# Performance work log

Hardware: AMD Instinct MI355X
Metric: run time of the kernel (lower is better)

The kernel has to match this reference:

```python
import jax, jax.numpy as jnp
import numpy as np

B, N, D, H = 2, 512, 256, 8
HD = D // H
DFF = 4 * D
EPS = 1e-5


def layer_norm(x, g, b):
    m = jnp.mean(x, axis=-1, keepdims=True)
    v = jnp.mean(jnp.square(x - m), axis=-1, keepdims=True)
    return (x - m) * jax.lax.rsqrt(v + EPS) * g + b


def setup_inputs() -> dict:
    key = jax.random.key(0)
    ks = jax.random.split(key, 16)
    s = 0.02
    return {
        "node_features": jax.random.normal(ks[0], (B, N, D), jnp.float32),
        "edge_features": jax.random.normal(ks[1], (B, N, N, D), jnp.float32),
        "adjacency_mask": jax.random.randint(ks[2], (B, N, N), 0, 2, jnp.int32),
        "node_norm_g": jnp.ones((D,), jnp.float32),
        "node_norm_b": jnp.zeros((D,), jnp.float32),
        "edge_norm_g": jnp.ones((D,), jnp.float32),
        "edge_norm_b": jnp.zeros((D,), jnp.float32),
        "Wq": jax.random.normal(ks[3], (D, D), jnp.float32) * s,
        "bq": jnp.zeros((D,), jnp.float32),
        "Wk": jax.random.normal(ks[4], (D, D), jnp.float32) * s,
        "bk": jnp.zeros((D,), jnp.float32),
        "Wv": jax.random.normal(ks[5], (D, D), jnp.float32) * s,
        "bv": jnp.zeros((D,), jnp.float32),
        "Wo": jax.random.normal(ks[6], (D, D), jnp.float32) * s,
        "bo": jnp.zeros((D,), jnp.float32),
        "We": jax.random.normal(ks[7], (D, H), jnp.float32) * s,
        "be": jnp.zeros((H,), jnp.float32),
        "ff_norm_g": jnp.ones((D,), jnp.float32),
        "ff_norm_b": jnp.zeros((D,), jnp.float32),
        "W1": jax.random.normal(ks[8], (D, DFF), jnp.float32) * s,
        "b1": jnp.zeros((DFF,), jnp.float32),
        "W2": jax.random.normal(ks[9], (DFF, D), jnp.float32) * s,
        "b2": jnp.zeros((D,), jnp.float32),
    }


def reference(node_features, edge_features, adjacency_mask,
              node_norm_g, node_norm_b, edge_norm_g, edge_norm_b,
              Wq, bq, Wk, bk, Wv, bv, Wo, bo, We, be,
              ff_norm_g, ff_norm_b, W1, b1, W2, b2):
    x = node_features
    nn_ = layer_norm(x, node_norm_g, node_norm_b)
    # project and split heads: (B, H, N, HD)
    q = (nn_ @ Wq + bq).reshape(B, N, H, HD).transpose(0, 2, 1, 3)
    k = (nn_ @ Wk + bk).reshape(B, N, H, HD).transpose(0, 2, 1, 3)
    v = (nn_ @ Wv + bv).reshape(B, N, H, HD).transpose(0, 2, 1, 3)
    scores = jnp.einsum('bhnd,bhmd->bhnm', q, k) / jnp.sqrt(jnp.float32(HD))
    # edge bias: LayerNorm over D then Linear(D->H), move H first
    eb = layer_norm(edge_features, edge_norm_g, edge_norm_b) @ We + be  # (B,N,N,H)
    scores = scores + eb.transpose(0, 3, 1, 2)
    scores = jnp.where(adjacency_mask[:, None, :, :] == 0, -jnp.inf, scores)
    attn = jax.nn.softmax(scores, axis=-1)
    out = jnp.einsum('bhnm,bhmd->bhnd', attn, v)
    out = out.transpose(0, 2, 1, 3).reshape(B, N, D) @ Wo + bo
    x = x + out
    # feedforward (dropout is identity at inference)
    h = layer_norm(x, ff_norm_g, ff_norm_b)
    h = jax.nn.gelu(h @ W1 + b1, approximate=False) @ W2 + b2
    return x + h
```

## Files before the change

### kernel.cpp

```cpp
#include <hip/hip_runtime.h>
#include <hip/hip_bf16.h>

typedef unsigned int uint;

constexpr float EPS_ = 1e-5f;

#define DEV __device__ __forceinline__

DEV float gelu_(float x){ return 0.5f*x*(1.f + erff(x*0.70710678118654752f)); }

__global__ __launch_bounds__(256) void k_setup(
    const float* __restrict__ g, const float* __restrict__ b,
    const float* __restrict__ We, const float* __restrict__ be,
    float* __restrict__ GW, float* __restrict__ A, float* __restrict__ C)
{
    const int d = threadIdx.x;
    __shared__ float redA[256*8];
    __shared__ float redC[256*8];
    float gd = g[d], bd = b[d];
    #pragma unroll
    for (int h = 0; h < 8; ++h) {
        float w = We[d*8+h];
        float gw = gd*w;
        GW[d*8+h] = gw;
        redA[d*8+h] = gw;
        redC[d*8+h] = bd*w;
    }
    __syncthreads();
    for (int s = 128; s >= 1; s >>= 1) {
        if (d < s) {
            #pragma unroll
            for (int h = 0; h < 8; ++h) {
                redA[d*8+h] += redA[(d+s)*8+h];
                redC[d*8+h] += redC[(d+s)*8+h];
            }
        }
        __syncthreads();
    }
    if (d < 8) {
        A[d] = redA[d];
        C[d] = redC[d] + be[d];
    }
}

__global__ __launch_bounds__(256) void k_qkv(
    const float* __restrict__ x,
    const float* __restrict__ g, const float* __restrict__ bta,
    const float* __restrict__ Wq, const float* __restrict__ bq,
    const float* __restrict__ Wk, const float* __restrict__ bk,
    const float* __restrict__ Wv, const float* __restrict__ bv,
    float* __restrict__ q, float* __restrict__ k, float* __restrict__ v)
{
    const int t = threadIdx.x;
    const int wid = t >> 6, l = t & 63;
    const int r0 = blockIdx.x << 1;
    __shared__ float sxT[256*2];
    if (wid < 2) {
        const int row = r0 + wid;
        const float4 xv4 = ((const float4*)x)[row*64 + l];
        float s  = xv4.x + xv4.y + xv4.z + xv4.w;
        float q2 = xv4.x*xv4.x + xv4.y*xv4.y + xv4.z*xv4.z + xv4.w*xv4.w;
        #pragma unroll
        for (int o = 32; o >= 1; o >>= 1) { s += __shfl_xor(s, o); q2 += __shfl_xor(q2, o); }
        const float m = s * (1.f/256.f);
        const float rinv = rsqrtf(q2*(1.f/256.f) - m*m + EPS_);
        const float4 g4 = ((const float4*)g)[l];
        const float4 b4 = ((const float4*)bta)[l];
        sxT[(4*l+0)*2 + wid] = (xv4.x - m)*rinv*g4.x + b4.x;
        sxT[(4*l+1)*2 + wid] = (xv4.y - m)*rinv*g4.y + b4.y;
        sxT[(4*l+2)*2 + wid] = (xv4.z - m)*rinv*g4.z + b4.z;
        sxT[(4*l+3)*2 + wid] = (xv4.w - m)*rinv*g4.w + b4.w;
    }
    __syncthreads();
    float aq0 = bq[t], ak0 = bk[t], av0 = bv[t];
    float aq1 = aq0, ak1 = ak0, av1 = av0;
    for (int d = 0; d < 256; d += 2) {
        const float4 s4 = *((const float4*)&sxT[d*2]);
        const float wqa = Wq[d*256 + t], wqb = Wq[(d+1)*256 + t];
        const float wka = Wk[d*256 + t], wkb = Wk[(d+1)*256 + t];
        const float wva = Wv[d*256 + t], wvb = Wv[(d+1)*256 + t];
        aq0 = fmaf(s4.x, wqa, aq0); aq0 = fmaf(s4.z, wqb, aq0);
        aq1 = fmaf(s4.y, wqa, aq1); aq1 = fmaf(s4.w, wqb, aq1);
        ak0 = fmaf(s4.x, wka, ak0); ak0 = fmaf(s4.z, wkb, ak0);
        ak1 = fmaf(s4.y, wka, ak1); ak1 = fmaf(s4.w, wkb, ak1);
        av0 = fmaf(s4.x, wva, av0); av0 = fmaf(s4.z, wvb, av0);
        av1 = fmaf(s4.y, wva, av1); av1 = fmaf(s4.w, wvb, av1);
    }
    q[(r0+0)*256 + t] = aq0; q[(r0+1)*256 + t] = aq1;
    k[(r0+0)*256 + t] = ak0; k[(r0+1)*256 + t] = ak1;
    v[(r0+0)*256 + t] = av0; v[(r0+1)*256 + t] = av1;
}

__global__ __launch_bounds__(256) void k_eattn(
    const float4* __restrict__ ep,
    const int*   __restrict__ msk,
    const float* __restrict__ GWg, const float* __restrict__ Avec, const float* __restrict__ Cvec,
    const float* __restrict__ qg, const float4* __restrict__ kg4, const float* __restrict__ vg,
    float* __restrict__ ao)
{
    __shared__ float slds[256*20];
    __shared__ float sb[8*512];
    __shared__ float sqv[256];
    __shared__ float sden[8];
    const int t = threadIdx.x;
    const int bi = blockIdx.x;
    const int b = bi >> 9;
    sqv[t] = qg[(size_t)bi*256 + t] * 0.17677669529663687f;
    __syncthreads();

    for (int half = 0; half < 2; ++half) {
        const long long rowBase = ((long long)bi << 9) + (half << 8);
        const int krow0 = (b << 9) + (half << 8);
        float sum = 0.f, ssq = 0.f;
        float S[8]  = {0.f,0.f,0.f,0.f,0.f,0.f,0.f,0.f};
        float qk[8] = {0.f,0.f,0.f,0.f,0.f,0.f,0.f,0.f};

        for (int c = 0; c < 16; ++c) {
            #pragma unroll
            for (int kk = 0; kk < 4; ++kk) {
                const int l2 = (kk << 8) + t;
                const int r = l2 >> 2, u = l2 & 3;
                *((float4*)&slds[r*20 + (u << 2)]) = ep[(rowBase + r)*64 + (c << 2) + u];
            }
            __syncthreads();
            const float* srow = &slds[t*20];
            const int d0 = c << 4;
            #pragma unroll
            for (int j4 = 0; j4 < 4; ++j4) {
                const float4 e4 = *((const float4*)&srow[j4 << 2]);
                #pragma unroll
                for (int u = 0; u < 4; ++u) {
                    const float e = (u==0) ? e4.x : (u==1) ? e4.y : (u==2) ? e4.z : e4.w;
                    const float* gw = &GWg[(size_t)(d0 + (j4 << 2) + u) << 3];
                    sum += e;
                    ssq = fmaf(e, e, ssq);
                    S[0] = fmaf(e, gw[0], S[0]); S[1] = fmaf(e, gw[1], S[1]);
                    S[2] = fmaf(e, gw[2], S[2]); S[3] = fmaf(e, gw[3], S[3]);
                    S[4] = fmaf(e, gw[4], S[4]); S[5] = fmaf(e, gw[5], S[5]);
                    S[6] = fmaf(e, gw[6], S[6]); S[7] = fmaf(e, gw[7], S[7]);
                }
            }
            __syncthreads();
        }

        for (int c = 0; c < 16; ++c) {
            #pragma unroll
            for (int kk = 0; kk < 4; ++kk) {
                const int l2 = (kk << 8) + t;
                const int r = l2 >> 2, u = l2 & 3;
                *((float4*)&slds[r*20 + (u << 2)]) = kg4[(size_t)(krow0 + r)*64 + (c << 2) + u];
            }
            __syncthreads();
            const float* srow = &slds[t*20];
            const float4* q4p = (const float4*)&sqv[c << 4];
            float acc = qk[c >> 1];
            #pragma unroll
            for (int j4 = 0; j4 < 4; ++j4) {
                const float4 k4 = *((const float4*)&srow[j4 << 2]);
                const float4 q4 = q4p[j4];
                acc = fmaf(k4.x, q4.x, acc); acc = fmaf(k4.y, q4.y, acc);
                acc = fmaf(k4.z, q4.z, acc); acc = fmaf(k4.w, q4.w, acc);
            }
            qk[c >> 1] = acc;
            __syncthreads();
        }

        const float m = sum * (1.f/256.f);
        const float rinv = rsqrtf(ssq*(1.f/256.f) - m*m + EPS_);
        const float mb = (msk[rowBase + t] == 0) ? -1e30f : 0.f;
        const int jrow = (half << 8) + t;
        #pragma unroll
        for (int h = 0; h < 8; ++h)
            sb[h*512 + jrow] = qk[h] + rinv * (S[h] - m * Avec[h]) + Cvec[h] + mb;
    }
    __syncthreads();

    {
        const int h = t >> 5, l = t & 31;
        float* base = &sb[h*512 + (l << 4)];
        float4 s4[4];
        float pmax = -3.0e38f;
        #pragma unroll
        for (int i = 0; i < 4; ++i) {
            s4[i] = *((const float4*)&base[i << 2]);
            pmax = fmaxf(pmax, fmaxf(fmaxf(s4[i].x, s4[i].y), fmaxf(s4[i].z, s4[i].w)));
        }
        #pragma unroll
        for (int o = 16; o >= 1; o >>= 1) pmax = fmaxf(pmax, __shfl_xor(pmax, o));
        float psum = 0.f;
        #pragma unroll
        for (int i = 0; i < 4; ++i) {
            const float p0 = __expf(s4[i].x - pmax), p1 = __expf(s4[i].y - pmax);
            const float p2 = __expf(s4[i].z - pmax), p3 = __expf(s4[i].w - pmax);
            psum += (p0 + p1) + (p2 + p3);
            *((float4*)&base[i << 2]) = make_float4(p0, p1, p2, p3);
        }
        #pragma unroll
        for (int o = 16; o >= 1; o >>= 1) psum += __shfl_xor(psum, o);
        if (l == 0) sden[h] = psum;
    }
    __syncthreads();

    {
        const int h = t >> 5;
        const float* vb = vg + ((size_t)b << 9)*256 + t;
        const float4* spr4 = (const float4*)&sb[h*512];
        float a0 = 0.f, a1 = 0.f, a2 = 0.f, a3 = 0.f;
        for (int j4 = 0; j4 < 128; ++j4) {
            const float4 p4 = spr4[j4];
            const float* vj = vb + ((size_t)j4 << 2)*256;
            a0 = fmaf(p4.x, vj[0],   a0);
            a1 = fmaf(p4.y, vj[256], a1);
            a2 = fmaf(p4.z, vj[512], a2);
            a3 = fmaf(p4.w, vj[768], a3);
        }
        ao[(size_t)bi*256 + t] = (a0+a1+a2+a3) / sden[h];
    }
}

__global__ __launch_bounds__(256) void k_proj(
    const float* __restrict__ at, const float* __restrict__ Wo,
    const float* __restrict__ bo, const float* __restrict__ x,
    float* __restrict__ x1)
{
    const int t = threadIdx.x;
    const int wid = t >> 6, l = t & 63;
    const int r0 = blockIdx.x << 1;
    __shared__ float saT[256*2];
    if (wid < 2) {
        const float4 a4 = ((const float4*)at)[(r0 + wid)*64 + l];
        saT[(4*l+0)*2 + wid] = a4.x;
        saT[(4*l+1)*2 + wid] = a4.y;
        saT[(4*l+2)*2 + wid] = a4.z;
        saT[(4*l+3)*2 + wid] = a4.w;
    }
    __syncthreads();
    float A0 = bo[t], A1 = A0;
    for (int d = 0; d < 256; d += 2) {
        const float4 s4 = *((const float4*)&saT[d*2]);
        const float wa = Wo[d*256 + t], wb = Wo[(d+1)*256 + t];
        A0 = fmaf(s4.x, wa, A0); A0 = fmaf(s4.z, wb, A0);
        A1 = fmaf(s4.y, wa, A1); A1 = fmaf(s4.w, wb, A1);
    }
    x1[(r0+0)*256 + t] = A0 + x[(r0+0)*256 + t];
    x1[(r0+1)*256 + t] = A1 + x[(r0+1)*256 + t];
}

__global__ __launch_bounds__(256) void k_ff(
    const float* __restrict__ x1, const float* __restrict__ g,
    const float* __restrict__ bb,
    const float* __restrict__ W1, const float* __restrict__ b1,
    const float* __restrict__ W2, const float* __restrict__ b2,
    float* __restrict__ out)
{
    const int t = threadIdx.x;
    const int wid = t >> 6, l = t & 63;
    const int r0 = blockIdx.x << 2;
    __shared__ float shT[256*4];
    __shared__ float sfT[1024*4];
    {
        const int row = r0 + wid;
        const float4 xv4 = ((const float4*)x1)[row*64 + l];
        float s  = xv4.x + xv4.y + xv4.z + xv4.w;
        float q2 = xv4.x*xv4.x + xv4.y*xv4.y + xv4.z*xv4.z + xv4.w*xv4.w;
        #pragma unroll
        for (int o = 32; o >= 1; o >>= 1) { s += __shfl_xor(s, o); q2 += __shfl_xor(q2, o); }
        const float m = s * (1.f/256.f);
        const float rinv = rsqrtf(q2*(1.f/256.f) - m*m + EPS_);
        const float4 g4 = ((const float4*)g)[l];
        const float4 b4 = ((const float4*)bb)[l];
        shT[(4*l+0)*4 + wid] = (xv4.x - m)*rinv*g4.x + b4.x;
        shT[(4*l+1)*4 + wid] = (xv4.y - m)*rinv*g4.y + b4.y;
        shT[(4*l+2)*4 + wid] = (xv4.z - m)*rinv*g4.z + b4.z;
        shT[(4*l+3)*4 + wid] = (xv4.w - m)*rinv*g4.w + b4.w;
    }
    __syncthreads();
    const float4 bc = ((const float4*)b1)[t];
    float4 Ac0 = make_float4(bc.x,bc.x,bc.x,bc.x);
    float4 Ac1 = make_float4(bc.y,bc.y,bc.y,bc.y);
    float4 Ac2 = make_float4(bc.z,bc.z,bc.z,bc.z);
    float4 Ac3 = make_float4(bc.w,bc.w,bc.w,bc.w);
    const float4* W14 = (const float4*)W1;
    for (int d = 0; d < 256; ++d) {
        const float4 s4 = *((const float4*)&shT[d*4]);
        const float4 w4 = W14[d*256 + t];
        Ac0.x = fmaf(s4.x, w4.x, Ac0.x); Ac0.y = fmaf(s4.y, w4.x, Ac0.y);
        Ac0.z = fmaf(s4.z, w4.x, Ac0.z); Ac0.w = fmaf(s4.w, w4.x, Ac0.w);
        Ac1.x = fmaf(s4.x, w4.y, Ac1.x); Ac1.y = fmaf(s4.y, w4.y, Ac1.y);
        Ac1.z = fmaf(s4.z, w4.y, Ac1.z); Ac1.w = fmaf(s4.w, w4.y, Ac1.w);
        Ac2.x = fmaf(s4.x, w4.z, Ac2.x); Ac2.y = fmaf(s4.y, w4.z, Ac2.y);
        Ac2.z = fmaf(s4.z, w4.z, Ac2.z); Ac2.w = fmaf(s4.w, w4.z, Ac2.w);
        Ac3.x = fmaf(s4.x, w4.w, Ac3.x); Ac3.y = fmaf(s4.y, w4.w, Ac3.y);
        Ac3.z = fmaf(s4.z, w4.w, Ac3.z); Ac3.w = fmaf(s4.w, w4.w, Ac3.w);
    }
    *((float4*)&sfT[(4*t+0)*4]) = make_float4(gelu_(Ac0.x), gelu_(Ac0.y), gelu_(Ac0.z), gelu_(Ac0.w));
    *((float4*)&sfT[(4*t+1)*4]) = make_float4(gelu_(Ac1.x), gelu_(Ac1.y), gelu_(Ac1.z), gelu_(Ac1.w));
    *((float4*)&sfT[(4*t+2)*4]) = make_float4(gelu_(Ac2.x), gelu_(Ac2.y), gelu_(Ac2.z), gelu_(Ac2.w));
    *((float4*)&sfT[(4*t+3)*4]) = make_float4(gelu_(Ac3.x), gelu_(Ac3.y), gelu_(Ac3.z), gelu_(Ac3.w));
    __syncthreads();
    const float b2v = b2[t];
    float4 AO = make_float4(b2v,b2v,b2v,b2v);
    for (int kk = 0; kk < 1024; ++kk) {
        const float4 s4 = *((const float4*)&sfT[kk*4]);
        const float w = W2[kk*256 + t];
        AO.x = fmaf(s4.x, w, AO.x); AO.y = fmaf(s4.y, w, AO.y);
        AO.z = fmaf(s4.z, w, AO.z); AO.w = fmaf(s4.w, w, AO.w);
    }
    out[(r0+0)*256 + t] = AO.x + x1[(r0+0)*256 + t];
    out[(r0+1)*256 + t] = AO.y + x1[(r0+1)*256 + t];
    out[(r0+2)*256 + t] = AO.z + x1[(r0+2)*256 + t];
    out[(r0+3)*256 + t] = AO.w + x1[(r0+3)*256 + t];
}

extern "C" void kernel_launch(void* const* d_in, const int* in_sizes, int n_in,
                              void* d_out, int out_size, void* d_ws, size_t ws_size,
                              hipStream_t stream) {
    const float* x   = (const float*)d_in[0];
    const float* ef  = (const float*)d_in[1];
    const int*   am  = (const int*)d_in[2];
    const float* ng  = (const float*)d_in[3];
    const float* nb  = (const float*)d_in[4];
    const float* eg  = (const float*)d_in[5];
    const float* ebb = (const float*)d_in[6];
    const float* Wq  = (const float*)d_in[7];
    const float* bq  = (const float*)d_in[8];
    const float* Wk  = (const float*)d_in[9];
    const float* bk  = (const float*)d_in[10];
    const float* Wv  = (const float*)d_in[11];
    const float* bv  = (const float*)d_in[12];
    const float* Wo  = (const float*)d_in[13];
    const float* bo  = (const float*)d_in[14];
    const float* We  = (const float*)d_in[15];
    const float* be  = (const float*)d_in[16];
    const float* fg  = (const float*)d_in[17];
    const float* fb  = (const float*)d_in[18];
    const float* W1  = (const float*)d_in[19];
    const float* b1  = (const float*)d_in[20];
    const float* W2  = (const float*)d_in[21];
    const float* b2  = (const float*)d_in[22];

    float* ws  = (float*)d_ws;
    float* GW  = ws;
    float* Av  = ws + 2048;
    float* Cv  = ws + 2064;
    float* q   = ws + 4096;
    float* k   = q  + 262144;
    float* v   = k  + 262144;
    float* ao  = v  + 262144;
    float* x1  = ao + 262144;

    hipLaunchKernelGGL(k_setup, dim3(1), dim3(256), 0, stream, eg, ebb, We, be, GW, Av, Cv);
    hipLaunchKernelGGL(k_qkv, dim3(512), dim3(256), 0, stream,
                       x, ng, nb, Wq, bq, Wk, bk, Wv, bv, q, k, v);
    hipLaunchKernelGGL(k_eattn, dim3(1024), dim3(256), 0, stream,
                       (const float4*)ef, am, GW, Av, Cv, q, (const float4*)k, v, ao);
    hipLaunchKernelGGL(k_proj, dim3(512), dim3(256), 0, stream, ao, Wo, bo, x, x1);
    hipLaunchKernelGGL(k_ff, dim3(256), dim3(256), 0, stream,
                       x1, fg, fb, W1, b1, W2, b2, (float*)d_out);
}
```

Before: 293.0 us.

## Prefetch next edge/key chunk into registers while computing current chunk

Merges the edge-feature and key loops into one 32-step loop and software-pipelines the global loads. Each step issues the next chunk's float4 loads into registers before computing on the current LDS tile, so global latency overlaps the FMA work. The cost is extra live registers and a per-iteration branch, which could reduce occupancy.

Result: no change. 291.6 us (-0.5%).

```diff
diff --git a/kernel.cpp b/kernel.cpp
--- a/kernel.cpp
+++ b/kernel.cpp
@@ -108,6 +108,8 @@
     sqv[t] = qg[(size_t)bi*256 + t] * 0.17677669529663687f;
     __syncthreads();
 
+    const int r = t >> 2, u = t & 3;
+
     for (int half = 0; half < 2; ++half) {
         const long long rowBase = ((long long)bi << 9) + (half << 8);
         const int krow0 = (b << 9) + (half << 8);
@@ -115,53 +117,65 @@
         float S[8]  = {0.f,0.f,0.f,0.f,0.f,0.f,0.f,0.f};
         float qk[8] = {0.f,0.f,0.f,0.f,0.f,0.f,0.f,0.f};
 
-        for (int c = 0; c < 16; ++c) {
-            #pragma unroll
-            for (int kk = 0; kk < 4; ++kk) {
-                const int l2 = (kk << 8) + t;
-                const int r = l2 >> 2, u = l2 & 3;
-                *((float4*)&slds[r*20 + (u << 2)]) = ep[(rowBase + r)*64 + (c << 2) + u];
-            }
+        float4 R0, R1, R2, R3;
+        {
+            R0 = ep[(rowBase + r      )*64 + u];
+            R1 = ep[(rowBase + r +  64)*64 + u];
+            R2 = ep[(rowBase + r + 128)*64 + u];
+            R3 = ep[(rowBase + r + 192)*64 + u];
+        }
+        for (int cc = 0; cc < 32; ++cc) {
+            *((float4*)&slds[(r      )*20 + (u << 2)]) = R0;
+            *((float4*)&slds[(r +  64)*20 + (u << 2)]) = R1;
+            *((float4*)&slds[(r + 128)*20 + (u << 2)]) = R2;
+            *((float4*)&slds[(r + 192)*20 + (u << 2)]) = R3;
             __syncthreads();
-            const float* srow = &slds[t*20];
-            const int d0 = c << 4;
-            #pragma unroll
-            for (int j4 = 0; j4 < 4; ++j4) {
-                const float4 e4 = *((const float4*)&srow[j4 << 2]);
-                #pragma unroll
-                for (int u = 0; u < 4; ++u) {
-                    const float e = (u==0) ? e4.x : (u==1) ? e4.y : (u==2) ? e4.z : e4.w;
-                    const float* gw = &GWg[(size_t)(d0 + (j4 << 2) + u) << 3];
-                    sum += e;
-                    ssq = fmaf(e, e, ssq);
-                    S[0] = fmaf(e, gw[0], S[0]); S[1] = fmaf(e, gw[1], S[1]);
-                    S[2] = fmaf(e, gw[2], S[2]); S[3] = fmaf(e, gw[3], S[3]);
-                    S[4] = fmaf(e, gw[4], S[4]); S[5] = fmaf(e, gw[5], S[5]);
-                    S[6] = fmaf(e, gw[6], S[6]); S[7] = fmaf(e, gw[7], S[7]);
+            if (cc + 1 < 32) {
+                const int nc = cc + 1;
+                if (nc < 16) {
+                    R0 = ep[(rowBase + r      )*64 + (nc << 2) + u];
+                    R1 = ep[(rowBase + r +  64)*64 + (nc << 2) + u];
+                    R2 = ep[(rowBase + r + 128)*64 + (nc << 2) + u];
+                    R3 = ep[(rowBase + r + 192)*64 + (nc << 2) + u];
+                } else {
+                    const int kc = nc - 16;
+                    R0 = kg4[(size_t)(krow0 + r      )*64 + (kc << 2) + u];
+                    R1 = kg4[(size_t)(krow0 + r +  64)*64 + (kc << 2) + u];
+                    R2 = kg4[(size_t)(krow0 + r + 128)*64 + (kc << 2) + u];
+                    R3 = kg4[(size_t)(krow0 + r + 192)*64 + (kc << 2) + u];
                 }
             }
-            __syncthreads();
-        }
-
-        for (int c = 0; c < 16; ++c) {
-            #pragma unroll
-            for (int kk = 0; kk < 4; ++kk) {
-                const int l2 = (kk << 8) + t;
-                const int r = l2 >> 2, u = l2 & 3;
-                *((float4*)&slds[r*20 + (u << 2)]) = kg4[(size_t)(krow0 + r)*64 + (c << 2) + u];
+            const float* srow = &slds[t*20];
+            if (cc < 16) {
+                const int d0 = cc << 4;
+                #pragma unroll
+                for (int j4 = 0; j4 < 4; ++j4) {
+                    const float4 e4 = *((const float4*)&srow[j4 << 2]);
+                    #pragma unroll
+                    for (int uu = 0; uu < 4; ++uu) {
+                        const float e = (uu==0) ? e4.x : (uu==1) ? e4.y : (uu==2) ? e4.z : e4.w;
+                        const float* gw = &GWg[(size_t)(d0 + (j4 << 2) + uu) << 3];
+                        sum += e;
+                        ssq = fmaf(e, e, ssq);
+                        S[0] = fmaf(e, gw[0], S[0]); S[1] = fmaf(e, gw[1], S[1]);
+                        S[2] = fmaf(e, gw[2], S[2]); S[3] = fmaf(e, gw[3], S[3]);
+                        S[4] = fmaf(e, gw[4], S[4]); S[5] = fmaf(e, gw[5], S[5]);
+                        S[6] = fmaf(e, gw[6], S[6]); S[7] = fmaf(e, gw[7], S[7]);
+                    }
+                }
+            } else {
+                const int kc = cc - 16;
+                const float4* q4p = (const float4*)&sqv[kc << 4];
+                float acc = qk[kc >> 1];
+                #pragma unroll
+                for (int j4 = 0; j4 < 4; ++j4) {
+                    const float4 k4 = *((const float4*)&srow[j4 << 2]);
+                    const float4 q4 = q4p[j4];
+                    acc = fmaf(k4.x, q4.x, acc); acc = fmaf(k4.y, q4.y, acc);
+                    acc = fmaf(k4.z, q4.z, acc); acc = fmaf(k4.w, q4.w, acc);
+                }
+                qk[kc >> 1] = acc;
             }
-            __syncthreads();
-            const float* srow = &slds[t*20];
-            const float4* q4p = (const float4*)&sqv[c << 4];
-            float acc = qk[c >> 1];
-            #pragma unroll
-            for (int j4 = 0; j4 < 4; ++j4) {
-                const float4 k4 = *((const float4*)&srow[j4 << 2]);
-                const float4 q4 = q4p[j4];
-                acc = fmaf(k4.x, q4.x, acc); acc = fmaf(k4.y, q4.y, acc);
-                acc = fmaf(k4.z, q4.z, acc); acc = fmaf(k4.w, q4.w, acc);
-            }
-            qk[c >> 1] = acc;
             __syncthreads();
         }
 
@@ -172,8 +186,8 @@
         #pragma unroll
         for (int h = 0; h < 8; ++h)
             sb[h*512 + jrow] = qk[h] + rinv * (S[h] - m * Avec[h]) + Cvec[h] + mb;
-    }
-    __syncthreads();
+        __syncthreads();
+    }
 
     {
         const int h = t >> 5, l = t & 31;
```

## Fold setup into QKV kernel, fuse proj+FF, share LDS in edge attention

Applied to the files above, without the earlier changes.

The one-block setup kernel is folded into block 0 of the QKV kernel, using a wave-shuffle reduction instead of a shared-memory tree. The output projection and feedforward kernels are fused so x1 stays in LDS, with the FF now processing 2 rows per block instead of 4. In the edge-attention kernel, the staging buffer and the score buffer share one LDS array and launch bounds request 5 blocks per CU, aiming for higher occupancy. Risks: fewer rows per block in the FF doubles the W1/W2 weight reads, and the S/qk state from both halves is now held in registers at the same time.

Result: faster. 271.8 us (median of 3 runs) (-7.2%).

```diff
diff --git a/kernel.cpp b/kernel.cpp
--- a/kernel.cpp
+++ b/kernel.cpp
@@ -8,40 +8,6 @@
 #define DEV __device__ __forceinline__
 
 DEV float gelu_(float x){ return 0.5f*x*(1.f + erff(x*0.70710678118654752f)); }
-
-__global__ __launch_bounds__(256) void k_setup(
-    const float* __restrict__ g, const float* __restrict__ b,
-    const float* __restrict__ We, const float* __restrict__ be,
-    float* __restrict__ GW, float* __restrict__ A, float* __restrict__ C)
-{
-    const int d = threadIdx.x;
-    __shared__ float redA[256*8];
-    __shared__ float redC[256*8];
-    float gd = g[d], bd = b[d];
-    #pragma unroll
-    for (int h = 0; h < 8; ++h) {
-        float w = We[d*8+h];
-        float gw = gd*w;
-        GW[d*8+h] = gw;
-        redA[d*8+h] = gw;
-        redC[d*8+h] = bd*w;
-    }
-    __syncthreads();
-    for (int s = 128; s >= 1; s >>= 1) {
-        if (d < s) {
-            #pragma unroll
-            for (int h = 0; h < 8; ++h) {
-                redA[d*8+h] += redA[(d+s)*8+h];
-                redC[d*8+h] += redC[(d+s)*8+h];
-            }
-        }
-        __syncthreads();
-    }
-    if (d < 8) {
-        A[d] = redA[d];
-        C[d] = redC[d] + be[d];
-    }
-}
 
 __global__ __launch_bounds__(256) void k_qkv(
     const float* __restrict__ x,
@@ -49,9 +15,45 @@
     const float* __restrict__ Wq, const float* __restrict__ bq,
     const float* __restrict__ Wk, const float* __restrict__ bk,
     const float* __restrict__ Wv, const float* __restrict__ bv,
+    const float* __restrict__ eg, const float* __restrict__ ebb,
+    const float* __restrict__ We, const float* __restrict__ be,
+    float* __restrict__ GW, float* __restrict__ Av, float* __restrict__ Cv,
     float* __restrict__ q, float* __restrict__ k, float* __restrict__ v)
 {
     const int t = threadIdx.x;
+    __shared__ float redA2[4][8];
+    __shared__ float redC2[4][8];
+    if (blockIdx.x == 0) {
+        float gd = eg[t], bd = ebb[t];
+        float a_loc[8], c_loc[8];
+        #pragma unroll
+        for (int h = 0; h < 8; ++h) {
+            float w = We[t*8 + h];
+            float gw = gd * w;
+            GW[t*8 + h] = gw;
+            a_loc[h] = gw;
+            c_loc[h] = bd * w;
+        }
+        #pragma unroll
+        for (int h = 0; h < 8; ++h) {
+            #pragma unroll
+            for (int o = 32; o >= 1; o >>= 1) {
+                a_loc[h] += __shfl_xor(a_loc[h], o);
+                c_loc[h] += __shfl_xor(c_loc[h], o);
+            }
+        }
+        if ((t & 63) == 0) {
+            const int w = t >> 6;
+            #pragma unroll
+            for (int h = 0; h < 8; ++h) { redA2[w][h] = a_loc[h]; redC2[w][h] = c_loc[h]; }
+        }
+        __syncthreads();
+        if (t < 8) {
+            Av[t] = redA2[0][t] + redA2[1][t] + redA2[2][t] + redA2[3][t];
+            Cv[t] = redC2[0][t] + redC2[1][t] + redC2[2][t] + redC2[3][t] + be[t];
+        }
+    }
+
     const int wid = t >> 6, l = t & 63;
     const int r0 = blockIdx.x << 1;
     __shared__ float sxT[256*2];
@@ -91,15 +93,14 @@
     v[(r0+0)*256 + t] = av0; v[(r0+1)*256 + t] = av1;
 }
 
-__global__ __launch_bounds__(256) void k_eattn(
+__global__ __launch_bounds__(256, 5) void k_eattn(
     const float4* __restrict__ ep,
     const int*   __restrict__ msk,
     const float* __restrict__ GWg, const float* __restrict__ Avec, const float* __restrict__ Cvec,
     const float* __restrict__ qg, const float4* __restrict__ kg4, const float* __restrict__ vg,
     float* __restrict__ ao)
 {
-    __shared__ float slds[256*20];
-    __shared__ float sb[8*512];
+    __shared__ float smem[5120];
     __shared__ float sqv[256];
     __shared__ float sden[8];
     const int t = threadIdx.x;
@@ -108,52 +109,53 @@
     sqv[t] = qg[(size_t)bi*256 + t] * 0.17677669529663687f;
     __syncthreads();
 
+    const int r = t >> 2, u = t & 3;
+
+    float S[2][8], qk[2][8], mval[2], rinv[2], mb[2];
+
+    #pragma unroll
     for (int half = 0; half < 2; ++half) {
         const long long rowBase = ((long long)bi << 9) + (half << 8);
         const int krow0 = (b << 9) + (half << 8);
         float sum = 0.f, ssq = 0.f;
-        float S[8]  = {0.f,0.f,0.f,0.f,0.f,0.f,0.f,0.f};
-        float qk[8] = {0.f,0.f,0.f,0.f,0.f,0.f,0.f,0.f};
+        #pragma unroll
+        for (int h = 0; h < 8; ++h) { S[half][h] = 0.f; qk[half][h] = 0.f; }
 
         for (int c = 0; c < 16; ++c) {
-            #pragma unroll
-            for (int kk = 0; kk < 4; ++kk) {
-                const int l2 = (kk << 8) + t;
-                const int r = l2 >> 2, u = l2 & 3;
-                *((float4*)&slds[r*20 + (u << 2)]) = ep[(rowBase + r)*64 + (c << 2) + u];
-            }
+            *((float4*)&smem[(r      )*20 + (u << 2)]) = ep[(rowBase + r      )*64 + (c << 2) + u];
+            *((float4*)&smem[(r +  64)*20 + (u << 2)]) = ep[(rowBase + r +  64)*64 + (c << 2) + u];
+            *((float4*)&smem[(r + 128)*20 + (u << 2)]) = ep[(rowBase + r + 128)*64 + (c << 2) + u];
+            *((float4*)&smem[(r + 192)*20 + (u << 2)]) = ep[(rowBase + r + 192)*64 + (c << 2) + u];
             __syncthreads();
-            const float* srow = &slds[t*20];
+            const float* srow = &smem[t*20];
             const int d0 = c << 4;
             #pragma unroll
             for (int j4 = 0; j4 < 4; ++j4) {
                 const float4 e4 = *((const float4*)&srow[j4 << 2]);
                 #pragma unroll
-                for (int u = 0; u < 4; ++u) {
-                    const float e = (u==0) ? e4.x : (u==1) ? e4.y : (u==2) ? e4.z : e4.w;
-                    const float* gw = &GWg[(size_t)(d0 + (j4 << 2) + u) << 3];
+                for (int uu = 0; uu < 4; ++uu) {
+                    const float e = (uu==0) ? e4.x : (uu==1) ? e4.y : (uu==2) ? e4.z : e4.w;
+                    const float* gw = &GWg[(size_t)(d0 + (j4 << 2) + uu) << 3];
                     sum += e;
                     ssq = fmaf(e, e, ssq);
-                    S[0] = fmaf(e, gw[0], S[0]); S[1] = fmaf(e, gw[1], S[1]);
-                    S[2] = fmaf(e, gw[2], S[2]); S[3] = fmaf(e, gw[3], S[3]);
-                    S[4] = fmaf(e, gw[4], S[4]); S[5] = fmaf(e, gw[5], S[5]);
-                    S[6] = fmaf(e, gw[6], S[6]); S[7] = fmaf(e, gw[7], S[7]);
+                    S[half][0] = fmaf(e, gw[0], S[half][0]); S[half][1] = fmaf(e, gw[1], S[half][1]);
+                    S[half][2] = fmaf(e, gw[2], S[half][2]); S[half][3] = fmaf(e, gw[3], S[half][3]);
+                    S[half][4] = fmaf(e, gw[4], S[half][4]); S[half][5] = fmaf(e, gw[5], S[half][5]);
+                    S[half][6] = fmaf(e, gw[6], S[half][6]); S[half][7] = fmaf(e, gw[7], S[half][7]);
                 }
             }
             __syncthreads();
         }
 
         for (int c = 0; c < 16; ++c) {
-            #pragma unroll
-            for (int kk = 0; kk < 4; ++kk) {
-                const int l2 = (kk << 8) + t;
-                const int r = l2 >> 2, u = l2 & 3;
-                *((float4*)&slds[r*20 + (u << 2)]) = kg4[(size_t)(krow0 + r)*64 + (c << 2) + u];
-            }
+            *((float4*)&smem[(r      )*20 + (u << 2)]) = kg4[(size_t)(krow0 + r      )*64 + (c << 2) + u];
+            *((float4*)&smem[(r +  64)*20 + (u << 2)]) = kg4[(size_t)(krow0 + r +  64)*64 + (c << 2) + u];
+            *((float4*)&smem[(r + 128)*20 + (u << 2)]) = kg4[(size_t)(krow0 + r + 128)*64 + (c << 2) + u];
+            *((float4*)&smem[(r + 192)*20 + (u << 2)]) = kg4[(size_t)(krow0 + r + 192)*64 + (c << 2) + u];
             __syncthreads();
-            const float* srow = &slds[t*20];
+            const float* srow = &smem[t*20];
             const float4* q4p = (const float4*)&sqv[c << 4];
-            float acc = qk[c >> 1];
+            float acc = qk[half][c >> 1];
             #pragma unroll
             for (int j4 = 0; j4 < 4; ++j4) {
                 const float4 k4 = *((const float4*)&srow[j4 << 2]);
@@ -161,17 +163,24 @@
                 acc = fmaf(k4.x, q4.x, acc); acc = fmaf(k4.y, q4.y, acc);
                 acc = fmaf(k4.z, q4.z, acc); acc = fmaf(k4.w, q4.w, acc);
             }
-            qk[c >> 1] = acc;
+            qk[half][c >> 1] = acc;
             __syncthreads();
         }
 
-        const float m = sum * (1.f/256.f);
-        const float rinv = rsqrtf(ssq*(1.f/256.f) - m*m + EPS_);
-        const float mb = (msk[rowBase + t] == 0) ? -1e30f : 0.f;
+        mval[half] = sum * (1.f/256.f);
+        rinv[half] = rsqrtf(ssq*(1.f/256.f) - mval[half]*mval[half] + EPS_);
+        mb[half]   = (msk[rowBase + t] == 0) ? -1e30f : 0.f;
+    }
+
+    float* sb = smem;
+    #pragma unroll
+    for (int half = 0; half < 2; ++half) {
         const int jrow = (half << 8) + t;
         #pragma unroll
         for (int h = 0; h < 8; ++h)
-            sb[h*512 + jrow] = qk[h] + rinv * (S[h] - m * Avec[h]) + Cvec[h] + mb;
+            sb[h*512 + jrow] = qk[half][h]
+                             + rinv[half] * (S[half][h] - mval[half] * Avec[h])
+                             + Cvec[h] + mb[half];
     }
     __syncthreads();
 
@@ -218,15 +227,22 @@
     }
 }
 
-__global__ __launch_bounds__(256) void k_proj(
+__global__ __launch_bounds__(256) void k_projff(
     const float* __restrict__ at, const float* __restrict__ Wo,
     const float* __restrict__ bo, const float* __restrict__ x,
-    float* __restrict__ x1)
+    const float* __restrict__ g, const float* __restrict__ bb,
+    const float* __restrict__ W1, const float* __restrict__ b1,
+    const float* __restrict__ W2, const float* __restrict__ b2,
+    float* __restrict__ out)
 {
     const int t = threadIdx.x;
     const int wid = t >> 6, l = t & 63;
     const int r0 = blockIdx.x << 1;
     __shared__ float saT[256*2];
+    __shared__ float shT[256*2];
+    __shared__ float sfT[2*1024];
+    __shared__ float sx1[2][256];
+
     if (wid < 2) {
         const float4 a4 = ((const float4*)at)[(r0 + wid)*64 + l];
         saT[(4*l+0)*2 + wid] = a4.x;
@@ -235,32 +251,20 @@
         saT[(4*l+3)*2 + wid] = a4.w;
     }
     __syncthreads();
-    float A0 = bo[t], A1 = A0;
-    for (int d = 0; d < 256; d += 2) {
-        const float4 s4 = *((const float4*)&saT[d*2]);
-        const float wa = Wo[d*256 + t], wb = Wo[(d+1)*256 + t];
-        A0 = fmaf(s4.x, wa, A0); A0 = fmaf(s4.z, wb, A0);
-        A1 = fmaf(s4.y, wa, A1); A1 = fmaf(s4.w, wb, A1);
-    }
-    x1[(r0+0)*256 + t] = A0 + x[(r0+0)*256 + t];
-    x1[(r0+1)*256 + t] = A1 + x[(r0+1)*256 + t];
-}
-
-__global__ __launch_bounds__(256) void k_ff(
-    const float* __restrict__ x1, const float* __restrict__ g,
-    const float* __restrict__ bb,
-    const float* __restrict__ W1, const float* __restrict__ b1,
-    const float* __restrict__ W2, const float* __restrict__ b2,
-    float* __restrict__ out)
-{
-    const int t = threadIdx.x;
-    const int wid = t >> 6, l = t & 63;
-    const int r0 = blockIdx.x << 2;
-    __shared__ float shT[256*4];
-    __shared__ float sfT[1024*4];
-    {
-        const int row = r0 + wid;
-        const float4 xv4 = ((const float4*)x1)[row*64 + l];
+    {
+        float A0 = bo[t], A1 = A0;
+        for (int d = 0; d < 256; d += 2) {
+            const float4 s4 = *((const float4*)&saT[d*2]);
+            const float wa = Wo[d*256 + t], wb = Wo[(d+1)*256 + t];
+            A0 = fmaf(s4.x, wa, A0); A0 = fmaf(s4.z, wb, A0);
+            A1 = fmaf(s4.y, wa, A1); A1 = fmaf(s4.w, wb, A1);
+        }
+        sx1[0][t] = A0 + x[(r0+0)*256 + t];
+        sx1[1][t] = A1 + x[(r0+1)*256 + t];
+    }
+    __syncthreads();
+    if (wid < 2) {
+        const float4 xv4 = *((const float4*)&sx1[wid][4*l]);
         float s  = xv4.x + xv4.y + xv4.z + xv4.w;
         float q2 = xv4.x*xv4.x + xv4.y*xv4.y + xv4.z*xv4.z + xv4.w*xv4.w;
         #pragma unroll
@@ -269,47 +273,41 @@
         const float rinv = rsqrtf(q2*(1.f/256.f) - m*m + EPS_);
         const float4 g4 = ((const float4*)g)[l];
         const float4 b4 = ((const float4*)bb)[l];
-        shT[(4*l+0)*4 + wid] = (xv4.x - m)*rinv*g4.x + b4.x;
-        shT[(4*l+1)*4 + wid] = (xv4.y - m)*rinv*g4.y + b4.y;
-        shT[(4*l+2)*4 + wid] = (xv4.z - m)*rinv*g4.z + b4.z;
-        shT[(4*l+3)*4 + wid] = (xv4.w - m)*rinv*g4.w + b4.w;
-    }
-    __syncthreads();
-    const float4 bc = ((const float4*)b1)[t];
-    float4 Ac0 = make_float4(bc.x,bc.x,bc.x,bc.x);
-    float4 Ac1 = make_float4(bc.y,bc.y,bc.y,bc.y);
-    float4 Ac2 = make_float4(bc.z,bc.z,bc.z,bc.z);
-    float4 Ac3 = make_float4(bc.w,bc.w,bc.w,bc.w);
-    const float4* W14 = (const float4*)W1;
-    for (int d = 0; d < 256; ++d) {
-        const float4 s4 = *((const float4*)&shT[d*4]);
-        const float4 w4 = W14[d*256 + t];
-        Ac0.x = fmaf(s4.x, w4.x, Ac0.x); Ac0.y = fmaf(s4.y, w4.x, Ac0.y);
-        Ac0.z = fmaf(s4.z, w4.x, Ac0.z); Ac0.w = fmaf(s4.w, w4.x, Ac0.w);
-        Ac1.x = fmaf(s4.x, w4.y, Ac1.x); Ac1.y = fmaf(s4.y, w4.y, Ac1.y);
-        Ac1.z = fmaf(s4.z, w4.y, Ac1.z); Ac1.w = fmaf(s4.w, w4.y, Ac1.w);
-        Ac2.x = fmaf(s4.x, w4.z, Ac2.x); Ac2.y = fmaf(s4.y, w4.z, Ac2.y);
-        Ac2.z = fmaf(s4.z, w4.z, Ac2.z); Ac2.w = fmaf(s4.w, w4.z, Ac2.w);
-        Ac3.x = fmaf(s4.x, w4.w, Ac3.x); Ac3.y = fmaf(s4.y, w4.w, Ac3.y);
-        Ac3.z = fmaf(s4.z, w4.w, Ac3.z); Ac3.w = fmaf(s4.w, w4.w, Ac3.w);
-    }
-    *((float4*)&sfT[(4*t+0)*4]) = make_float4(gelu_(Ac0.x), gelu_(Ac0.y), gelu_(Ac0.z), gelu_(Ac0.w));
-    *((float4*)&sfT[(4*t+1)*4]) = make_float4(gelu_(Ac1.x), gelu_(Ac1.y), gelu_(Ac1.z), gelu_(Ac1.w));
-    *((float4*)&sfT[(4*t+2)*4]) = make_float4(gelu_(Ac2.x), gelu_(Ac2.y), gelu_(Ac2.z), gelu_(Ac2.w));
-    *((float4*)&sfT[(4*t+3)*4]) = make_float4(gelu_(Ac3.x), gelu_(Ac3.y), gelu_(Ac3.z), gelu_(Ac3.w));
-    __syncthreads();
-    const float b2v = b2[t];
-    float4 AO = make_float4(b2v,b2v,b2v,b2v);
-    for (int kk = 0; kk < 1024; ++kk) {
-        const float4 s4 = *((const float4*)&sfT[kk*4]);
-        const float w = W2[kk*256 + t];
-        AO.x = fmaf(s4.x, w, AO.x); AO.y = fmaf(s4.y, w, AO.y);
-        AO.z = fmaf(s4.z, w, AO.z); AO.w = fmaf(s4.w, w, AO.w);
-    }
-    out[(r0+0)*256 + t] = AO.x + x1[(r0+0)*256 + t];
-    out[(r0+1)*256 + t] = AO.y + x1[(r0+1)*256 + t];
-    out[(r0+2)*256 + t] = AO.z + x1[(r0+2)*256 + t];
-    out[(r0+3)*256 + t] = AO.w + x1[(r0+3)*256 + t];
+        shT[(4*l+0)*2 + wid] = (xv4.x - m)*rinv*g4.x + b4.x;
+        shT[(4*l+1)*2 + wid] = (xv4.y - m)*rinv*g4.y + b4.y;
+        shT[(4*l+2)*2 + wid] = (xv4.z - m)*rinv*g4.z + b4.z;
+        shT[(4*l+3)*2 + wid] = (xv4.w - m)*rinv*g4.w + b4.w;
+    }
+    __syncthreads();
+    {
+        const float4 bc = ((const float4*)b1)[t];
+        float A00 = bc.x, A01 = bc.x;
+        float A10 = bc.y, A11 = bc.y;
+        float A20 = bc.z, A21 = bc.z;
+        float A30 = bc.w, A31 = bc.w;
+        const float4* W14 = (const float4*)W1;
+        for (int d = 0; d < 256; ++d) {
+            const float2 s2 = *((const float2*)&shT[d*2]);
+            const float4 w4 = W14[d*256 + t];
+            A00 = fmaf(s2.x, w4.x, A00); A01 = fmaf(s2.y, w4.x, A01);
+            A10 = fmaf(s2.x, w4.y, A10); A11 = fmaf(s2.y, w4.y, A11);
+            A20 = fmaf(s2.x, w4.z, A20); A21 = fmaf(s2.y, w4.z, A21);
+            A30 = fmaf(s2.x, w4.w, A30); A31 = fmaf(s2.y, w4.w, A31);
+        }
+        *((float4*)&sfT[0*1024 + 4*t]) = make_float4(gelu_(A00), gelu_(A10), gelu_(A20), gelu_(A30));
+        *((float4*)&sfT[1*1024 + 4*t]) = make_float4(gelu_(A01), gelu_(A11), gelu_(A21), gelu_(A31));
+    }
+    __syncthreads();
+    {
+        float AO0 = b2[t], AO1 = AO0;
+        for (int kk = 0; kk < 1024; ++kk) {
+            const float w = W2[kk*256 + t];
+            AO0 = fmaf(sfT[kk],        w, AO0);
+            AO1 = fmaf(sfT[1024 + kk], w, AO1);
+        }
+        out[(r0+0)*256 + t] = AO0 + sx1[0][t];
+        out[(r0+1)*256 + t] = AO1 + sx1[1][t];
+    }
 }
 
 extern "C" void kernel_launch(void* const* d_in, const int* in_sizes, int n_in,
@@ -347,14 +345,12 @@
     float* k   = q  + 262144;
     float* v   = k  + 262144;
     float* ao  = v  + 262144;
-    float* x1  = ao + 262144;
-
-    hipLaunchKernelGGL(k_setup, dim3(1), dim3(256), 0, stream, eg, ebb, We, be, GW, Av, Cv);
+
     hipLaunchKernelGGL(k_qkv, dim3(512), dim3(256), 0, stream,
-                       x, ng, nb, Wq, bq, Wk, bk, Wv, bv, q, k, v);
+                       x, ng, nb, Wq, bq, Wk, bk, Wv, bv,
+                       eg, ebb, We, be, GW, Av, Cv, q, k, v);
     hipLaunchKernelGGL(k_eattn, dim3(1024), dim3(256), 0, stream,
                        (const float4*)ef, am, GW, Av, Cv, q, (const float4*)k, v, ao);
-    hipLaunchKernelGGL(k_proj, dim3(512), dim3(256), 0, stream, ao, Wo, bo, x, x1);
-    hipLaunchKernelGGL(k_ff, dim3(256), dim3(256), 0, stream,
-                       x1, fg, fb, W1, b1, W2, b2, (float*)d_out);
+    hipLaunchKernelGGL(k_projff, dim3(512), dim3(256), 0, stream,
+                       ao, Wo, bo, x, fg, fb, W1, b1, W2, b2, (float*)d_out);
 }
```
